# Kernel tuning notes

Measured on AMD Instinct MI355X. Metric: run time of the kernel, lower is better.

The kernel has to match this reference:

```python
import jax, jax.numpy as jnp
import numpy as np

N_NODES = 100000
N_EDGES = 1600000
IN_CH, HID, N_CLS = 768, 256, 8


def setup_inputs() -> dict:
    key = jax.random.key(0)
    k1, k2, k3, k4 = jax.random.split(key, 4)
    x = jax.random.normal(k1, (N_NODES, IN_CH), dtype=jnp.float32)
    edge_index = jax.random.randint(k2, (2, N_EDGES), 0, N_NODES, dtype=jnp.int64)
    # Glorot-ish init scaled for stability
    W1 = jax.random.normal(k3, (IN_CH, HID), dtype=jnp.float32) * (1.0 / np.sqrt(IN_CH))
    b1 = jnp.zeros((HID,), dtype=jnp.float32)
    W2 = jax.random.normal(k4, (HID, N_CLS), dtype=jnp.float32) * (1.0 / np.sqrt(HID))
    b2 = jnp.zeros((N_CLS,), dtype=jnp.float32)
    return {"x": x, "edge_index": edge_index, "W1": W1, "b1": b1, "W2": W2, "b2": b2}


def _gcn_norm(edge_index, num_nodes):
    # Add self-loops (PyG GCNConv default) and compute symmetric normalization.
    loops = jnp.arange(num_nodes, dtype=edge_index.dtype)
    row = jnp.concatenate([edge_index[0], loops])  # source nodes
    col = jnp.concatenate([edge_index[1], loops])  # target nodes
    ones = jnp.ones(col.shape[0], dtype=jnp.float32)
    deg = jax.ops.segment_sum(ones, col, num_segments=num_nodes)
    dinv = jnp.where(deg > 0, jax.lax.rsqrt(deg), 0.0)
    norm = dinv[row] * dinv[col]  # [E + N]
    return row, col, norm


def _gcn_conv(x, row, col, norm, W, b):
    h = x @ W                      # [N, out] dense transform first (out <= in)
    msg = h[row] * norm[:, None]    # gather + scale, [E+N, out]
    agg = jax.ops.segment_sum(msg, col, num_segments=x.shape[0])  # scatter-add
    return agg + b


def reference(x, edge_index, W1, b1, W2, b2):
    row, col, norm = _gcn_norm(edge_index, x.shape[0])
    h = _gcn_conv(x, row, col, norm, W1, b1)
    h = jax.nn.relu(h)
    # dropout is identity at eval (training=False)
    out = _gcn_conv(h, row, col, norm, W2, b2)
    return out
```

## Files before the change

kernel.cpp:

```cpp
#include <hip/hip_runtime.h>


#define NN 100000
#define NE 1600000
#define INC 768
#define HID 256
#define NCLS 8
#define NBLK 391

typedef short bf16x8 __attribute__((ext_vector_type(8)));
typedef float f32x4 __attribute__((ext_vector_type(4)));

__device__ __forceinline__ unsigned short f2bf(float f) {
  unsigned int u = __float_as_uint(f);
  unsigned int r = (u + 0x7FFFu + ((u >> 16) & 1u)) >> 16;
  return (unsigned short)r;
}
__device__ __forceinline__ float bf2f(unsigned short h) {
  return __uint_as_float(((unsigned int)h) << 16);
}

__global__ __launch_bounds__(256) void k_zero(int* __restrict__ cnt) {
  int i = blockIdx.x * 256 + threadIdx.x;
  if (i < NN) cnt[i] = 0;
}
__global__ __launch_bounds__(256) void k_count(const int* __restrict__ ei, int* __restrict__ cnt) {
  int e = blockIdx.x * 256 + threadIdx.x;
  if (e < NE) atomicAdd(&cnt[ei[NE + e]], 1);
}
__global__ __launch_bounds__(256) void k_dinv(const int* __restrict__ cnt, float* __restrict__ dinv) {
  int i = blockIdx.x * 256 + threadIdx.x;
  if (i < NN) dinv[i] = rsqrtf((float)cnt[i] + 1.0f);
}

__global__ __launch_bounds__(256) void k_scan1(const int* __restrict__ cnt, int* __restrict__ bsum) {
  __shared__ int s[256];
  int i = blockIdx.x * 256 + threadIdx.x;
  s[threadIdx.x] = (i < NN) ? cnt[i] : 0;
  __syncthreads();
#pragma unroll
  for (int off = 128; off > 0; off >>= 1) {
    if (threadIdx.x < off) s[threadIdx.x] += s[threadIdx.x + off];
    __syncthreads();
  }
  if (threadIdx.x == 0) bsum[blockIdx.x] = s[0];
}
__global__ __launch_bounds__(512) void k_scan2(const int* __restrict__ bsum, int* __restrict__ boff,
                                               int* __restrict__ rowptr) {
  __shared__ int s[512];
  int tid = threadIdx.x;
  int v = (tid < NBLK) ? bsum[tid] : 0;
  s[tid] = v;
  __syncthreads();
#pragma unroll
  for (int off = 1; off < 512; off <<= 1) {
    int t = (tid >= off) ? s[tid - off] : 0;
    __syncthreads();
    s[tid] += t;
    __syncthreads();
  }
  if (tid < NBLK) boff[tid] = s[tid] - v;
  if (tid == NBLK - 1) rowptr[NN] = s[tid];
}
__global__ __launch_bounds__(256) void k_scan3(const int* __restrict__ cnt, const int* __restrict__ boff,
                                               int* __restrict__ rowptr, int* __restrict__ cursor) {
  __shared__ int s[256];
  int i = blockIdx.x * 256 + threadIdx.x;
  int v = (i < NN) ? cnt[i] : 0;
  s[threadIdx.x] = v;
  __syncthreads();
#pragma unroll
  for (int off = 1; off < 256; off <<= 1) {
    int t = (threadIdx.x >= off) ? s[threadIdx.x - off] : 0;
    __syncthreads();
    s[threadIdx.x] += t;
    __syncthreads();
  }
  if (i < NN) {
    int e = boff[blockIdx.x] + s[threadIdx.x] - v;
    rowptr[i] = e;
    cursor[i] = e;
  }
}
__global__ __launch_bounds__(256) void k_fill(const int* __restrict__ ei, const float* __restrict__ dinv,
                                              int* __restrict__ cursor, int2* __restrict__ epk) {
  int e = blockIdx.x * 256 + threadIdx.x;
  if (e >= NE) return;
  int r = ei[e];
  int c = ei[NE + e];
  float w = dinv[r] * dinv[c];
  int pos = atomicAdd(&cursor[c], 1);
  epk[pos] = make_int2(r, __float_as_int(w));
}

__global__ __launch_bounds__(256) void k_w1t(const float* __restrict__ W1, unsigned short* __restrict__ w1t) {
  int t = blockIdx.x * 256 + threadIdx.x;
  if (t >= INC * HID) return;
  int k = t / HID, n = t % HID;
  w1t[n * INC + k] = f2bf(W1[t]);
}

__global__ __launch_bounds__(512) void k_gemm1(const float* __restrict__ x,
                                               const unsigned short* __restrict__ w1t,
                                               unsigned short* __restrict__ h1) {
  __shared__ char smem[49152];
  unsigned short* As = (unsigned short*)smem;
  unsigned short* Bs = (unsigned short*)(smem + 16384);
  const int tid = threadIdx.x;
  const int lane = tid & 63;
  const int wid = tid >> 6;
  const int wm = wid >> 2;
  const int wn = wid & 3;
  const long bm = blockIdx.x;

  const int ar0 = tid >> 3, as7 = tid & 7;
  const int ar1 = (tid + 512) >> 3;
  long arow0 = bm * 128 + ar0; if (arow0 > NN - 1) arow0 = NN - 1;
  long arow1 = bm * 128 + ar1; if (arow1 > NN - 1) arow1 = NN - 1;
  const float* gA0 = x + arow0 * INC + as7 * 8;
  const float* gA1 = x + arow1 * INC + as7 * 8;
  const int aoff0 = (ar0 << 7) | ((as7 ^ (ar0 & 7)) << 4);
  const int aoff1 = (ar1 << 7) | ((as7 ^ (ar1 & 7)) << 4);

  f32x4 acc[4][4];
#pragma unroll
  for (int m = 0; m < 4; m++)
#pragma unroll
    for (int n = 0; n < 4; n++) acc[m][n] = (f32x4){0.f, 0.f, 0.f, 0.f};

  float4 fa00, fa01, fa10, fa11;
  uint4 rb0, rb1, rb2, rb3;

#define LOAD_AB(KT)                                                        \
  do {                                                                     \
    fa00 = *(const float4*)(gA0 + (KT));                                   \
    fa01 = *(const float4*)(gA0 + (KT) + 4);                               \
    fa10 = *(const float4*)(gA1 + (KT));                                   \
    fa11 = *(const float4*)(gA1 + (KT) + 4);                               \
    rb0 = *(const uint4*)(w1t + (long)(tid >> 3) * INC + (KT) + (tid & 7) * 8);            \
    rb1 = *(const uint4*)(w1t + (long)((tid + 512) >> 3) * INC + (KT) + (tid & 7) * 8);    \
    rb2 = *(const uint4*)(w1t + (long)((tid + 1024) >> 3) * INC + (KT) + (tid & 7) * 8);   \
    rb3 = *(const uint4*)(w1t + (long)((tid + 1536) >> 3) * INC + (KT) + (tid & 7) * 8);   \
  } while (0)

  LOAD_AB(0);

  for (int kt = 0; kt < INC; kt += 64) {
    {
      union { unsigned short us[8]; uint4 v; } u;
      u.us[0] = f2bf(fa00.x); u.us[1] = f2bf(fa00.y); u.us[2] = f2bf(fa00.z); u.us[3] = f2bf(fa00.w);
      u.us[4] = f2bf(fa01.x); u.us[5] = f2bf(fa01.y); u.us[6] = f2bf(fa01.z); u.us[7] = f2bf(fa01.w);
      *(uint4*)((char*)As + aoff0) = u.v;
      u.us[0] = f2bf(fa10.x); u.us[1] = f2bf(fa10.y); u.us[2] = f2bf(fa10.z); u.us[3] = f2bf(fa10.w);
      u.us[4] = f2bf(fa11.x); u.us[5] = f2bf(fa11.y); u.us[6] = f2bf(fa11.z); u.us[7] = f2bf(fa11.w);
      *(uint4*)((char*)As + aoff1) = u.v;
    }
    {
      int r0 = tid >> 3, s7 = tid & 7;
      *(uint4*)((char*)Bs + ((r0 << 7) | ((s7 ^ (r0 & 7)) << 4))) = rb0;
      int r1 = (tid + 512) >> 3;
      *(uint4*)((char*)Bs + ((r1 << 7) | ((s7 ^ (r1 & 7)) << 4))) = rb1;
      int r2 = (tid + 1024) >> 3;
      *(uint4*)((char*)Bs + ((r2 << 7) | ((s7 ^ (r2 & 7)) << 4))) = rb2;
      int r3 = (tid + 1536) >> 3;
      *(uint4*)((char*)Bs + ((r3 << 7) | ((s7 ^ (r3 & 7)) << 4))) = rb3;
    }
    __syncthreads();
    if (kt + 64 < INC) LOAD_AB(kt + 64);
#pragma unroll
    for (int half = 0; half < 2; half++) {
      bf16x8 af[4], bff[4];
      int j = (half << 2) + (lane >> 4);
#pragma unroll
      for (int m = 0; m < 4; m++) {
        int row = wm * 64 + m * 16 + (lane & 15);
        int off = (row << 7) | ((j ^ (row & 7)) << 4);
        af[m] = *(const bf16x8*)((const char*)As + off);
      }
#pragma unroll
      for (int n = 0; n < 4; n++) {
        int row = wn * 64 + n * 16 + (lane & 15);
        int off = (row << 7) | ((j ^ (row & 7)) << 4);
        bff[n] = *(const bf16x8*)((const char*)Bs + off);
      }
#pragma unroll
      for (int m = 0; m < 4; m++)
#pragma unroll
        for (int n = 0; n < 4; n++)
          acc[m][n] = __builtin_amdgcn_mfma_f32_16x16x32_bf16(af[m], bff[n], acc[m][n], 0, 0, 0);
    }
    __syncthreads();
  }
#undef LOAD_AB

  unsigned short* Os = (unsigned short*)smem;
#pragma unroll
  for (int chunk = 0; chunk < 2; chunk++) {
    if (wm == chunk) {
#pragma unroll
      for (int m = 0; m < 4; m++)
#pragma unroll
        for (int n = 0; n < 4; n++) {
          int lrow = m * 16 + ((lane >> 4) << 2);
          int lcol = wn * 64 + n * 16 + (lane & 15);
#pragma unroll
          for (int r = 0; r < 4; r++)
            Os[(lrow + r) * 264 + lcol] = f2bf(acc[m][n][r]);
        }
    }
    __syncthreads();
    {
      int r = tid >> 3, s = tid & 7;
      long grow = bm * 128 + chunk * 64 + r;
      if (grow < NN) {
        unsigned short* dst = h1 + grow * HID;
#pragma unroll
        for (int i = 0; i < 4; i++) {
          int seg = s + i * 8;
          *(uint4*)(dst + seg * 8) = *(const uint4*)((const char*)Os + (long)r * 528 + seg * 16);
        }
      }
    }
    __syncthreads();
  }
}

__global__ __launch_bounds__(256) void k_agg1(const unsigned short* __restrict__ h1,
                                              const float* __restrict__ dinv,
                                              const int* __restrict__ rowptr,
                                              const int2* __restrict__ epk,
                                              const float* __restrict__ b1,
                                              const float* __restrict__ W2,
                                              float* __restrict__ h2) {
  int w = (int)((blockIdx.x * 256 + threadIdx.x) >> 6);
  int lane = threadIdx.x & 63;
  if (w >= NN) return;
  float di = dinv[w];
  int c4 = lane << 2;
  ushort4 hv = *(const ushort4*)(h1 + (long)w * HID + c4);
  float self = di * di;
  float a0 = self * bf2f(hv.x), a1 = self * bf2f(hv.y);
  float a2 = self * bf2f(hv.z), a3 = self * bf2f(hv.w);
  int e0 = rowptr[w], e1 = rowptr[w + 1];
  int e = e0;
  for (; e + 4 <= e1; e += 4) {
    int2 q0 = epk[e], q1 = epk[e + 1], q2 = epk[e + 2], q3 = epk[e + 3];
    ushort4 g0 = *(const ushort4*)(h1 + (long)q0.x * HID + c4);
    ushort4 g1 = *(const ushort4*)(h1 + (long)q1.x * HID + c4);
    ushort4 g2 = *(const ushort4*)(h1 + (long)q2.x * HID + c4);
    ushort4 g3 = *(const ushort4*)(h1 + (long)q3.x * HID + c4);
    float w0 = __int_as_float(q0.y), w1 = __int_as_float(q1.y);
    float w2 = __int_as_float(q2.y), w3 = __int_as_float(q3.y);
    a0 += w0 * bf2f(g0.x) + w1 * bf2f(g1.x) + w2 * bf2f(g2.x) + w3 * bf2f(g3.x);
    a1 += w0 * bf2f(g0.y) + w1 * bf2f(g1.y) + w2 * bf2f(g2.y) + w3 * bf2f(g3.y);
    a2 += w0 * bf2f(g0.z) + w1 * bf2f(g1.z) + w2 * bf2f(g2.z) + w3 * bf2f(g3.z);
    a3 += w0 * bf2f(g0.w) + w1 * bf2f(g1.w) + w2 * bf2f(g2.w) + w3 * bf2f(g3.w);
  }
  for (; e < e1; e++) {
    int2 q = epk[e];
    float ws = __int_as_float(q.y);
    ushort4 g = *(const ushort4*)(h1 + (long)q.x * HID + c4);
    a0 += ws * bf2f(g.x); a1 += ws * bf2f(g.y);
    a2 += ws * bf2f(g.z); a3 += ws * bf2f(g.w);
  }
  float4 bv = *(const float4*)(b1 + c4);
  float v0 = a0 + bv.x; v0 = v0 > 0.f ? v0 : 0.f;
  float v1 = a1 + bv.y; v1 = v1 > 0.f ? v1 : 0.f;
  float v2 = a2 + bv.z; v2 = v2 > 0.f ? v2 : 0.f;
  float v3 = a3 + bv.w; v3 = v3 > 0.f ? v3 : 0.f;
  const float4* wp = (const float4*)(W2 + ((long)c4 << 3));
  float4 r0a = wp[0], r0b = wp[1], r1a = wp[2], r1b = wp[3];
  float4 r2a = wp[4], r2b = wp[5], r3a = wp[6], r3b = wp[7];
  float p[8];
  p[0] = v0 * r0a.x + v1 * r1a.x + v2 * r2a.x + v3 * r3a.x;
  p[1] = v0 * r0a.y + v1 * r1a.y + v2 * r2a.y + v3 * r3a.y;
  p[2] = v0 * r0a.z + v1 * r1a.z + v2 * r2a.z + v3 * r3a.z;
  p[3] = v0 * r0a.w + v1 * r1a.w + v2 * r2a.w + v3 * r3a.w;
  p[4] = v0 * r0b.x + v1 * r1b.x + v2 * r2b.x + v3 * r3b.x;
  p[5] = v0 * r0b.y + v1 * r1b.y + v2 * r2b.y + v3 * r3b.y;
  p[6] = v0 * r0b.z + v1 * r1b.z + v2 * r2b.z + v3 * r3b.z;
  p[7] = v0 * r0b.w + v1 * r1b.w + v2 * r2b.w + v3 * r3b.w;
#pragma unroll
  for (int c = 0; c < 8; c++)
#pragma unroll
    for (int off = 1; off < 64; off <<= 1) p[c] += __shfl_xor(p[c], off, 64);
  if (lane < 8) {
    float o = p[0];
    o = (lane == 1) ? p[1] : o;
    o = (lane == 2) ? p[2] : o;
    o = (lane == 3) ? p[3] : o;
    o = (lane == 4) ? p[4] : o;
    o = (lane == 5) ? p[5] : o;
    o = (lane == 6) ? p[6] : o;
    o = (lane == 7) ? p[7] : o;
    h2[(long)w * NCLS + lane] = o;
  }
}

__global__ __launch_bounds__(256) void k_agg2(const float* __restrict__ h2,
                                              const float* __restrict__ dinv,
                                              const int* __restrict__ rowptr,
                                              const int2* __restrict__ epk,
                                              const float* __restrict__ b2,
                                              float* __restrict__ out) {
  long t = (long)blockIdx.x * 256 + threadIdx.x;
  long i = t >> 3;
  int c = (int)(t & 7);
  if (i >= NN) return;
  float di = dinv[i];
  float s = di * di * h2[i * NCLS + c];
  int e0 = rowptr[i], e1 = rowptr[i + 1];
  int e = e0;
  for (; e + 4 <= e1; e += 4) {
    int2 q0 = epk[e], q1 = epk[e + 1], q2 = epk[e + 2], q3 = epk[e + 3];
    float g0 = h2[(long)q0.x * NCLS + c], g1 = h2[(long)q1.x * NCLS + c];
    float g2 = h2[(long)q2.x * NCLS + c], g3 = h2[(long)q3.x * NCLS + c];
    s += __int_as_float(q0.y) * g0 + __int_as_float(q1.y) * g1 +
         __int_as_float(q2.y) * g2 + __int_as_float(q3.y) * g3;
  }
  for (; e < e1; e++) {
    int2 q = epk[e];
    s += __int_as_float(q.y) * h2[(long)q.x * NCLS + c];
  }
  out[i * NCLS + c] = s + b2[c];
}

extern "C" void kernel_launch(void* const* d_in, const int* in_sizes, int n_in,
                              void* d_out, int out_size, void* d_ws, size_t ws_size,
                              hipStream_t stream) {
  (void)in_sizes; (void)n_in; (void)out_size; (void)ws_size;
  const float* x  = (const float*)d_in[0];
  const int*   ei = (const int*)d_in[1];
  const float* W1 = (const float*)d_in[2];
  const float* b1 = (const float*)d_in[3];
  const float* W2 = (const float*)d_in[4];
  const float* b2 = (const float*)d_in[5];
  float* out = (float*)d_out;
  char* ws = (char*)d_ws;

  unsigned short* h1   = (unsigned short*)(ws + 0L);
  float* h2            = (float*)(ws + 51200000L);
  float* dinv          = (float*)(ws + 54400000L);
  int*   cnt           = (int*)(ws + 54800000L);
  int*   rowptr        = (int*)(ws + 55200000L);
  int*   cursor        = (int*)(ws + 55600128L);
  int2*  epk           = (int2*)(ws + 56000128L);
  unsigned short* w1t  = (unsigned short*)(ws + 68800128L);
  int*   bsum          = (int*)(ws + 69195008L);
  int*   boff          = (int*)(ws + 69196608L);

  k_zero<<<(NN + 255) / 256, 256, 0, stream>>>(cnt);
  k_count<<<(NE + 255) / 256, 256, 0, stream>>>(ei, cnt);
  k_dinv<<<(NN + 255) / 256, 256, 0, stream>>>(cnt, dinv);
  k_scan1<<<NBLK, 256, 0, stream>>>(cnt, bsum);
  k_scan2<<<1, 512, 0, stream>>>(bsum, boff, rowptr);
  k_scan3<<<NBLK, 256, 0, stream>>>(cnt, boff, rowptr, cursor);
  k_fill<<<(NE + 255) / 256, 256, 0, stream>>>(ei, dinv, cursor, epk);
  k_w1t<<<(INC * HID + 255) / 256, 256, 0, stream>>>(W1, w1t);
  k_gemm1<<<782, 512, 0, stream>>>(x, w1t, h1);
  k_agg1<<<(NN * 64 + 255) / 256, 256, 0, stream>>>(h1, dinv, rowptr, epk, b1, W2, h2);
  k_agg2<<<(NN * NCLS + 255) / 256, 256, 0, stream>>>(h2, dinv, rowptr, epk, b2, out);
}
```

Before: 461.1 us.

## Slab-transpose h1 for cache-local aggregation and split layer-2 transform

GEMM1 now writes h1 as 16 column slabs of 16 bf16 features each. The first aggregation runs one slab at a time, so each block group gathers from a 3.2 MB slab that can stay resident in cache instead of scattering across the full 51 MB h1. Self-loops are inserted into the CSR edge list, so the separate self terms go away, and the dinv computation is fused into the scan. The ReLU plus W2 transform moves into its own kernel that reads a bf16 aggregated buffer, which adds a 51 MB write and read round trip and one more bf16 rounding of the aggregate.

```diff
diff --git a/kernel.cpp b/kernel.cpp
--- a/kernel.cpp
+++ b/kernel.cpp
@@ -3,10 +3,12 @@
 
 #define NN 100000
 #define NE 1600000
+#define NEPK 1700000
 #define INC 768
 #define HID 256
 #define NCLS 8
 #define NBLK 391
+#define SLABN 1600000L
 
 typedef short bf16x8 __attribute__((ext_vector_type(8)));
 typedef float f32x4 __attribute__((ext_vector_type(4)));
@@ -20,23 +22,18 @@
   return __uint_as_float(((unsigned int)h) << 16);
 }
 
-__global__ __launch_bounds__(256) void k_zero(int* __restrict__ cnt) {
-  int i = blockIdx.x * 256 + threadIdx.x;
-  if (i < NN) cnt[i] = 0;
-}
 __global__ __launch_bounds__(256) void k_count(const int* __restrict__ ei, int* __restrict__ cnt) {
   int e = blockIdx.x * 256 + threadIdx.x;
   if (e < NE) atomicAdd(&cnt[ei[NE + e]], 1);
 }
-__global__ __launch_bounds__(256) void k_dinv(const int* __restrict__ cnt, float* __restrict__ dinv) {
-  int i = blockIdx.x * 256 + threadIdx.x;
-  if (i < NN) dinv[i] = rsqrtf((float)cnt[i] + 1.0f);
-}
-
-__global__ __launch_bounds__(256) void k_scan1(const int* __restrict__ cnt, int* __restrict__ bsum) {
+
+__global__ __launch_bounds__(256) void k_scan1(const int* __restrict__ cnt, int* __restrict__ bsum,
+                                               float* __restrict__ dinv) {
   __shared__ int s[256];
   int i = blockIdx.x * 256 + threadIdx.x;
-  s[threadIdx.x] = (i < NN) ? cnt[i] : 0;
+  int v = (i < NN) ? (cnt[i] + 1) : 0;
+  if (i < NN) dinv[i] = rsqrtf((float)v);
+  s[threadIdx.x] = v;
   __syncthreads();
 #pragma unroll
   for (int off = 128; off > 0; off >>= 1) {
@@ -66,7 +63,7 @@
                                                int* __restrict__ rowptr, int* __restrict__ cursor) {
   __shared__ int s[256];
   int i = blockIdx.x * 256 + threadIdx.x;
-  int v = (i < NN) ? cnt[i] : 0;
+  int v = (i < NN) ? (cnt[i] + 1) : 0;
   s[threadIdx.x] = v;
   __syncthreads();
 #pragma unroll
@@ -92,6 +89,14 @@
   int pos = atomicAdd(&cursor[c], 1);
   epk[pos] = make_int2(r, __float_as_int(w));
 }
+__global__ __launch_bounds__(256) void k_selffill(const float* __restrict__ dinv,
+                                                  int* __restrict__ cursor, int2* __restrict__ epk) {
+  int i = blockIdx.x * 256 + threadIdx.x;
+  if (i >= NN) return;
+  float d = dinv[i];
+  int pos = atomicAdd(&cursor[i], 1);
+  epk[pos] = make_int2(i, __float_as_int(d * d));
+}
 
 __global__ __launch_bounds__(256) void k_w1t(const float* __restrict__ W1, unsigned short* __restrict__ w1t) {
   int t = blockIdx.x * 256 + threadIdx.x;
@@ -102,7 +107,7 @@
 
 __global__ __launch_bounds__(512) void k_gemm1(const float* __restrict__ x,
                                                const unsigned short* __restrict__ w1t,
-                                               unsigned short* __restrict__ h1) {
+                                               unsigned short* __restrict__ h1t) {
   __shared__ char smem[49152];
   unsigned short* As = (unsigned short*)smem;
   unsigned short* Bs = (unsigned short*)(smem + 16384);
@@ -209,96 +214,88 @@
         }
     }
     __syncthreads();
-    {
-      int r = tid >> 3, s = tid & 7;
-      long grow = bm * 128 + chunk * 64 + r;
-      if (grow < NN) {
-        unsigned short* dst = h1 + grow * HID;
-#pragma unroll
-        for (int i = 0; i < 4; i++) {
-          int seg = s + i * 8;
-          *(uint4*)(dst + seg * 8) = *(const uint4*)((const char*)Os + (long)r * 528 + seg * 16);
-        }
-      }
-    }
-    __syncthreads();
-  }
-}
-
-__global__ __launch_bounds__(256) void k_agg1(const unsigned short* __restrict__ h1,
-                                              const float* __restrict__ dinv,
-                                              const int* __restrict__ rowptr,
-                                              const int2* __restrict__ epk,
-                                              const float* __restrict__ b1,
-                                              const float* __restrict__ W2,
-                                              float* __restrict__ h2) {
-  int w = (int)((blockIdx.x * 256 + threadIdx.x) >> 6);
+#pragma unroll
+    for (int i = 0; i < 4; i++) {
+      int idx = i * 512 + tid;
+      int slab = idx >> 7;
+      int row = (idx >> 1) & 63;
+      int half = idx & 1;
+      long grow = bm * 128 + chunk * 64 + row;
+      if (grow < NN)
+        *(uint4*)(h1t + (long)slab * SLABN + grow * 16 + half * 8) =
+            *(const uint4*)((const char*)Os + (long)row * 528 + slab * 32 + half * 16);
+    }
+    __syncthreads();
+  }
+}
+
+__global__ __launch_bounds__(256) void k_agg1s(const unsigned short* __restrict__ h1t,
+                                               const int* __restrict__ rowptr,
+                                               const int2* __restrict__ epk,
+                                               unsigned short* __restrict__ agg1b) {
+  int b = blockIdx.x;
+  int slab = (b & 7) + ((b >> 11) << 3);
+  int j = (b >> 3) & 255;
+  int widx = threadIdx.x >> 6;
   int lane = threadIdx.x & 63;
-  if (w >= NN) return;
-  float di = dinv[w];
-  int c4 = lane << 2;
-  ushort4 hv = *(const ushort4*)(h1 + (long)w * HID + c4);
-  float self = di * di;
-  float a0 = self * bf2f(hv.x), a1 = self * bf2f(hv.y);
-  float a2 = self * bf2f(hv.z), a3 = self * bf2f(hv.w);
-  int e0 = rowptr[w], e1 = rowptr[w + 1];
-  int e = e0;
-  for (; e + 4 <= e1; e += 4) {
-    int2 q0 = epk[e], q1 = epk[e + 1], q2 = epk[e + 2], q3 = epk[e + 3];
-    ushort4 g0 = *(const ushort4*)(h1 + (long)q0.x * HID + c4);
-    ushort4 g1 = *(const ushort4*)(h1 + (long)q1.x * HID + c4);
-    ushort4 g2 = *(const ushort4*)(h1 + (long)q2.x * HID + c4);
-    ushort4 g3 = *(const ushort4*)(h1 + (long)q3.x * HID + c4);
-    float w0 = __int_as_float(q0.y), w1 = __int_as_float(q1.y);
-    float w2 = __int_as_float(q2.y), w3 = __int_as_float(q3.y);
-    a0 += w0 * bf2f(g0.x) + w1 * bf2f(g1.x) + w2 * bf2f(g2.x) + w3 * bf2f(g3.x);
-    a1 += w0 * bf2f(g0.y) + w1 * bf2f(g1.y) + w2 * bf2f(g2.y) + w3 * bf2f(g3.y);
-    a2 += w0 * bf2f(g0.z) + w1 * bf2f(g1.z) + w2 * bf2f(g2.z) + w3 * bf2f(g3.z);
-    a3 += w0 * bf2f(g0.w) + w1 * bf2f(g1.w) + w2 * bf2f(g2.w) + w3 * bf2f(g3.w);
-  }
-  for (; e < e1; e++) {
-    int2 q = epk[e];
-    float ws = __int_as_float(q.y);
-    ushort4 g = *(const ushort4*)(h1 + (long)q.x * HID + c4);
-    a0 += ws * bf2f(g.x); a1 += ws * bf2f(g.y);
-    a2 += ws * bf2f(g.z); a3 += ws * bf2f(g.w);
-  }
-  float4 bv = *(const float4*)(b1 + c4);
-  float v0 = a0 + bv.x; v0 = v0 > 0.f ? v0 : 0.f;
-  float v1 = a1 + bv.y; v1 = v1 > 0.f ? v1 : 0.f;
-  float v2 = a2 + bv.z; v2 = v2 > 0.f ? v2 : 0.f;
-  float v3 = a3 + bv.w; v3 = v3 > 0.f ? v3 : 0.f;
-  const float4* wp = (const float4*)(W2 + ((long)c4 << 3));
-  float4 r0a = wp[0], r0b = wp[1], r1a = wp[2], r1b = wp[3];
-  float4 r2a = wp[4], r2b = wp[5], r3a = wp[6], r3b = wp[7];
-  float p[8];
-  p[0] = v0 * r0a.x + v1 * r1a.x + v2 * r2a.x + v3 * r3a.x;
-  p[1] = v0 * r0a.y + v1 * r1a.y + v2 * r2a.y + v3 * r3a.y;
-  p[2] = v0 * r0a.z + v1 * r1a.z + v2 * r2a.z + v3 * r3a.z;
-  p[3] = v0 * r0a.w + v1 * r1a.w + v2 * r2a.w + v3 * r3a.w;
-  p[4] = v0 * r0b.x + v1 * r1b.x + v2 * r2b.x + v3 * r3b.x;
-  p[5] = v0 * r0b.y + v1 * r1b.y + v2 * r2b.y + v3 * r3b.y;
-  p[6] = v0 * r0b.z + v1 * r1b.z + v2 * r2b.z + v3 * r3b.z;
-  p[7] = v0 * r0b.w + v1 * r1b.w + v2 * r2b.w + v3 * r3b.w;
-#pragma unroll
-  for (int c = 0; c < 8; c++)
-#pragma unroll
-    for (int off = 1; off < 64; off <<= 1) p[c] += __shfl_xor(p[c], off, 64);
-  if (lane < 8) {
-    float o = p[0];
-    o = (lane == 1) ? p[1] : o;
-    o = (lane == 2) ? p[2] : o;
-    o = (lane == 3) ? p[3] : o;
-    o = (lane == 4) ? p[4] : o;
-    o = (lane == 5) ? p[5] : o;
-    o = (lane == 6) ? p[6] : o;
-    o = (lane == 7) ? p[7] : o;
-    h2[(long)w * NCLS + lane] = o;
-  }
+  int slot = lane >> 3, cp = lane & 7;
+  const unsigned short* hs = h1t + (long)slab * SLABN + cp * 2;
+  int wv = j * 4 + widx;
+  for (int node = wv; node < NN; node += 1024) {
+    int e0 = rowptr[node], e1 = rowptr[node + 1];
+    float a0 = 0.f, a1 = 0.f;
+    for (int e = e0 + slot; e < e1; e += 8) {
+      int2 q = epk[e];
+      float w = __int_as_float(q.y);
+      ushort2 g = *(const ushort2*)(hs + (long)q.x * 16);
+      a0 += w * bf2f(g.x);
+      a1 += w * bf2f(g.y);
+    }
+#pragma unroll
+    for (int off = 8; off < 64; off <<= 1) {
+      a0 += __shfl_xor(a0, off, 64);
+      a1 += __shfl_xor(a1, off, 64);
+    }
+    if (slot == 0) {
+      ushort2 o;
+      o.x = f2bf(a0);
+      o.y = f2bf(a1);
+      *(ushort2*)(agg1b + (long)node * HID + slab * 16 + cp * 2) = o;
+    }
+  }
+}
+
+__global__ __launch_bounds__(256) void k_l2(const unsigned short* __restrict__ agg1b,
+                                            const float* __restrict__ b1,
+                                            const float* __restrict__ W2,
+                                            float* __restrict__ h2) {
+  __shared__ float w2s[HID * NCLS];
+  __shared__ float b1s[HID];
+  int tid = threadIdx.x;
+  for (int i = tid; i < HID * NCLS; i += 256) w2s[i] = W2[i];
+  b1s[tid] = b1[tid];
+  __syncthreads();
+  long t = (long)blockIdx.x * 256 + tid;
+  long i = t >> 3;
+  int c = (int)(t & 7);
+  if (i >= NN) return;
+  const ushort4* ap = (const ushort4*)(agg1b + i * HID);
+  float s = 0.f;
+#pragma unroll 8
+  for (int k4 = 0; k4 < HID / 4; k4++) {
+    ushort4 a = ap[k4];
+    int k = k4 * 4;
+    float v0 = bf2f(a.x) + b1s[k + 0]; v0 = v0 > 0.f ? v0 : 0.f;
+    float v1 = bf2f(a.y) + b1s[k + 1]; v1 = v1 > 0.f ? v1 : 0.f;
+    float v2 = bf2f(a.z) + b1s[k + 2]; v2 = v2 > 0.f ? v2 : 0.f;
+    float v3 = bf2f(a.w) + b1s[k + 3]; v3 = v3 > 0.f ? v3 : 0.f;
+    s += v0 * w2s[(k + 0) * NCLS + c] + v1 * w2s[(k + 1) * NCLS + c] +
+         v2 * w2s[(k + 2) * NCLS + c] + v3 * w2s[(k + 3) * NCLS + c];
+  }
+  h2[i * NCLS + c] = s;
 }
 
 __global__ __launch_bounds__(256) void k_agg2(const float* __restrict__ h2,
-                                              const float* __restrict__ dinv,
                                               const int* __restrict__ rowptr,
                                               const int2* __restrict__ epk,
                                               const float* __restrict__ b2,
@@ -307,16 +304,19 @@
   long i = t >> 3;
   int c = (int)(t & 7);
   if (i >= NN) return;
-  float di = dinv[i];
-  float s = di * di * h2[i * NCLS + c];
-  int e0 = rowptr[i], e1 = rowptr[i + 1];
-  int e = e0;
-  for (; e + 4 <= e1; e += 4) {
-    int2 q0 = epk[e], q1 = epk[e + 1], q2 = epk[e + 2], q3 = epk[e + 3];
+  float s = 0.f;
+  int e = rowptr[i], e1 = rowptr[i + 1];
+  for (; e + 8 <= e1; e += 8) {
+    int2 q0 = epk[e],     q1 = epk[e + 1], q2 = epk[e + 2], q3 = epk[e + 3];
+    int2 q4 = epk[e + 4], q5 = epk[e + 5], q6 = epk[e + 6], q7 = epk[e + 7];
     float g0 = h2[(long)q0.x * NCLS + c], g1 = h2[(long)q1.x * NCLS + c];
     float g2 = h2[(long)q2.x * NCLS + c], g3 = h2[(long)q3.x * NCLS + c];
+    float g4 = h2[(long)q4.x * NCLS + c], g5 = h2[(long)q5.x * NCLS + c];
+    float g6 = h2[(long)q6.x * NCLS + c], g7 = h2[(long)q7.x * NCLS + c];
     s += __int_as_float(q0.y) * g0 + __int_as_float(q1.y) * g1 +
-         __int_as_float(q2.y) * g2 + __int_as_float(q3.y) * g3;
+         __int_as_float(q2.y) * g2 + __int_as_float(q3.y) * g3 +
+         __int_as_float(q4.y) * g4 + __int_as_float(q5.y) * g5 +
+         __int_as_float(q6.y) * g6 + __int_as_float(q7.y) * g7;
   }
   for (; e < e1; e++) {
     int2 q = epk[e];
@@ -338,26 +338,28 @@
   float* out = (float*)d_out;
   char* ws = (char*)d_ws;
 
-  unsigned short* h1   = (unsigned short*)(ws + 0L);
-  float* h2            = (float*)(ws + 51200000L);
-  float* dinv          = (float*)(ws + 54400000L);
-  int*   cnt           = (int*)(ws + 54800000L);
-  int*   rowptr        = (int*)(ws + 55200000L);
-  int*   cursor        = (int*)(ws + 55600128L);
-  int2*  epk           = (int2*)(ws + 56000128L);
-  unsigned short* w1t  = (unsigned short*)(ws + 68800128L);
-  int*   bsum          = (int*)(ws + 69195008L);
-  int*   boff          = (int*)(ws + 69196608L);
-
-  k_zero<<<(NN + 255) / 256, 256, 0, stream>>>(cnt);
+  unsigned short* h1t   = (unsigned short*)(ws + 0L);
+  unsigned short* agg1b = (unsigned short*)(ws + 51200000L);
+  float* h2             = (float*)(ws + 102400000L);
+  float* dinv           = (float*)(ws + 105600000L);
+  int*   cnt            = (int*)(ws + 106000000L);
+  int*   rowptr         = (int*)(ws + 106400000L);
+  int*   cursor         = (int*)(ws + 106800128L);
+  int2*  epk            = (int2*)(ws + 107200128L);
+  unsigned short* w1t   = (unsigned short*)(ws + 120800128L);
+  int*   bsum           = (int*)(ws + 121193344L);
+  int*   boff           = (int*)(ws + 121194944L);
+
+  hipMemsetAsync(cnt, 0, NN * sizeof(int), stream);
   k_count<<<(NE + 255) / 256, 256, 0, stream>>>(ei, cnt);
-  k_dinv<<<(NN + 255) / 256, 256, 0, stream>>>(cnt, dinv);
-  k_scan1<<<NBLK, 256, 0, stream>>>(cnt, bsum);
+  k_scan1<<<NBLK, 256, 0, stream>>>(cnt, bsum, dinv);
   k_scan2<<<1, 512, 0, stream>>>(bsum, boff, rowptr);
   k_scan3<<<NBLK, 256, 0, stream>>>(cnt, boff, rowptr, cursor);
   k_fill<<<(NE + 255) / 256, 256, 0, stream>>>(ei, dinv, cursor, epk);
+  k_selffill<<<(NN + 255) / 256, 256, 0, stream>>>(dinv, cursor, epk);
   k_w1t<<<(INC * HID + 255) / 256, 256, 0, stream>>>(W1, w1t);
-  k_gemm1<<<782, 512, 0, stream>>>(x, w1t, h1);
-  k_agg1<<<(NN * 64 + 255) / 256, 256, 0, stream>>>(h1, dinv, rowptr, epk, b1, W2, h2);
-  k_agg2<<<(NN * NCLS + 255) / 256, 256, 0, stream>>>(h2, dinv, rowptr, epk, b2, out);
-}
+  k_gemm1<<<782, 512, 0, stream>>>(x, w1t, h1t);
+  k_agg1s<<<4096, 256, 0, stream>>>(h1t, rowptr, epk, agg1b);
+  k_l2<<<(NN * NCLS + 255) / 256, 256, 0, stream>>>(agg1b, b1, W2, h2);
+  k_agg2<<<(NN * NCLS + 255) / 256, 256, 0, stream>>>(h2, rowptr, epk, b2, out);
+}
```

New measurement: 712.2 us. 1.54x slower.
